# Kernel tuning notes

Hardware: AMD Instinct MI355X
Metric: run time of the kernel (lower is better)

Reference implementation:

```python
import jax, jax.numpy as jnp
import numpy as np

TEMPERATURE = 8.0  # sqrt(head_dim=64)
B, H, S, D = 4, 16, 2048, 64

def setup_inputs() -> dict:
    key = jax.random.key(0)
    kq, kk, kv, km = jax.random.split(key, 4)
    q = jax.random.normal(kq, (B, H, S, D), dtype=jnp.float32)
    k = jax.random.normal(kk, (B, H, S, D), dtype=jnp.float32)
    v = jax.random.normal(kv, (B, H, S, D), dtype=jnp.float32)
    # multiplicative 0/1 mask, broadcast over batch and heads
    mask = jax.random.randint(km, (1, 1, S, S), 0, 2).astype(jnp.float32)
    return {"q": q, "k": k, "v": v, "mask": mask}

def reference(q, k, v, mask):
    # attn = (q / T) @ k^T, multiplicatively masked, softmax over keys, then @ v
    attn = jnp.einsum("bhqd,bhkd->bhqk", q / TEMPERATURE, k)
    attn = attn * mask  # multiplicative mask (NOT additive -inf masking)
    attn = jax.nn.softmax(attn, axis=-1)
    return jnp.einsum("bhqk,bhkd->bhqd", attn, v)
```

## Files before the change

kernel.cpp:

```cpp
#include <hip/hip_runtime.h>
#include <hip/hip_bf16.h>


typedef __attribute__((ext_vector_type(4))) float  f32x4;
typedef __attribute__((ext_vector_type(8))) short  short8;
typedef __attribute__((ext_vector_type(4))) short  short4v;

constexpr int S = 2048, D = 64;
constexpr int NBH = 64;
constexpr int QBLK = 256, KT = 64;
constexpr int NQT = S / QBLK;
constexpr int NKT = S / KT;
constexpr float SCALE = 0.125f * 1.44269504088896340736f;
constexpr size_t TILE_SH = (size_t)KT * D;
constexpr size_t IMG_SH  = (size_t)NBH * NKT * TILE_SH;
constexpr size_t WS_NEED = 2 * IMG_SH * sizeof(short);

__device__ inline unsigned short bfb(float x) {
    union { __hip_bfloat16 h; unsigned short u; } cv;
    cv.h = __float2bfloat16(x);
    return cv.u;
}

__device__ inline float fexp2(float x) {
#if __has_builtin(__builtin_amdgcn_exp2f)
    return __builtin_amdgcn_exp2f(x);
#else
    return __expf(x * 0.6931471805599453f);
#endif
}

__device__ inline void gload16(const short* g, short* l) {
    auto gp = (const __attribute__((address_space(1))) int*)g;
    auto lp = (__attribute__((address_space(3))) int*)l;
    __builtin_amdgcn_global_load_lds(gp, lp, 16, 0, 0);
}

__global__ __launch_bounds__(256)
void conv_kv(const float* __restrict__ K, const float* __restrict__ V,
             short* __restrict__ Kimg, short* __restrict__ Vimg) {
    const int t = threadIdx.x;
    const int nt = NBH * NKT;
    if (blockIdx.x < nt) {
        const float* src = K + (size_t)blockIdx.x * TILE_SH;
        short* dst = Kimg + (size_t)blockIdx.x * TILE_SH;
        const int row = t >> 2, c16 = (t & 3) * 16;
        const int swz = (row & 7) << 3;
        float4 f0 = *reinterpret_cast<const float4*>(src + row * D + c16 + 0);
        float4 f1 = *reinterpret_cast<const float4*>(src + row * D + c16 + 4);
        float4 f2 = *reinterpret_cast<const float4*>(src + row * D + c16 + 8);
        float4 f3 = *reinterpret_cast<const float4*>(src + row * D + c16 + 12);
        short8 a, b;
        a[0]=bfb(f0.x); a[1]=bfb(f0.y); a[2]=bfb(f0.z); a[3]=bfb(f0.w);
        a[4]=bfb(f1.x); a[5]=bfb(f1.y); a[6]=bfb(f1.z); a[7]=bfb(f1.w);
        b[0]=bfb(f2.x); b[1]=bfb(f2.y); b[2]=bfb(f2.z); b[3]=bfb(f2.w);
        b[4]=bfb(f3.x); b[5]=bfb(f3.y); b[6]=bfb(f3.z); b[7]=bfb(f3.w);
        *reinterpret_cast<short8*>(dst + row * 64 + (c16 ^ swz)) = a;
        *reinterpret_cast<short8*>(dst + row * 64 + ((c16 + 8) ^ swz)) = b;
    } else {
        __shared__ float tl[64][65];
        const int blk = blockIdx.x - nt;
        const float* src = V + (size_t)blk * TILE_SH;
        short* dst = Vimg + (size_t)blk * TILE_SH;
        const int row = t >> 2, c16 = (t & 3) * 16;
        {
            float4 f0 = *reinterpret_cast<const float4*>(src + row * D + c16 + 0);
            float4 f1 = *reinterpret_cast<const float4*>(src + row * D + c16 + 4);
            float4 f2 = *reinterpret_cast<const float4*>(src + row * D + c16 + 8);
            float4 f3 = *reinterpret_cast<const float4*>(src + row * D + c16 + 12);
            tl[row][c16+0]=f0.x;  tl[row][c16+1]=f0.y;  tl[row][c16+2]=f0.z;  tl[row][c16+3]=f0.w;
            tl[row][c16+4]=f1.x;  tl[row][c16+5]=f1.y;  tl[row][c16+6]=f1.z;  tl[row][c16+7]=f1.w;
            tl[row][c16+8]=f2.x;  tl[row][c16+9]=f2.y;  tl[row][c16+10]=f2.z; tl[row][c16+11]=f2.w;
            tl[row][c16+12]=f3.x; tl[row][c16+13]=f3.y; tl[row][c16+14]=f3.z; tl[row][c16+15]=f3.w;
        }
        __syncthreads();
        const int d = t >> 2, k16 = (t & 3) * 16;
        const int swz = (d & 7) << 3;
        float vv[16];
#pragma unroll
        for (int j = 0; j < 16; ++j) vv[j] = tl[k16 + j][d];
        short8 a, b;
#pragma unroll
        for (int j = 0; j < 8; ++j) { a[j] = bfb(vv[j]); b[j] = bfb(vv[j + 8]); }
        *reinterpret_cast<short8*>(dst + d * 64 + (k16 ^ swz)) = a;
        *reinterpret_cast<short8*>(dst + d * 64 + ((k16 + 8) ^ swz)) = b;
    }
}

__global__ __launch_bounds__(512)
void attn_img(const float* __restrict__ Q, const float* __restrict__ M,
              const short* __restrict__ Kimg, const short* __restrict__ Vimg,
              float* __restrict__ O)
{
    __shared__ short Kb[3][4096];
    __shared__ short Vb[3][4096];
    __shared__ short Pt[8][16][64];

    const int tid  = threadIdx.x;
    const int w    = tid >> 6;
    const int lane = tid & 63;
    const int g    = lane >> 4;
    const int c    = lane & 15;
    const int swz8 = (c & 7) << 3;

    const int bid = blockIdx.x;
    const int bh  = bid >> 3;
    const int qt  = bid & 7;
    const int qw  = qt * QBLK + w * 32;

    const size_t bhS = (size_t)bh * S;
    const size_t bhT = (size_t)bh * NKT;

    short8 bQ[2][2];
#pragma unroll
    for (int rt = 0; rt < 2; ++rt) {
        const float* qp = Q + (bhS + qw + rt * 16 + c) * D;
#pragma unroll
        for (int kk = 0; kk < 2; ++kk) {
            const float* q8 = qp + kk * 32 + g * 8;
            float4 a = *reinterpret_cast<const float4*>(q8);
            float4 b = *reinterpret_cast<const float4*>(q8 + 4);
            short8 r;
            r[0] = bfb(a.x * SCALE); r[1] = bfb(a.y * SCALE);
            r[2] = bfb(a.z * SCALE); r[3] = bfb(a.w * SCALE);
            r[4] = bfb(b.x * SCALE); r[5] = bfb(b.y * SCALE);
            r[6] = bfb(b.z * SCALE); r[7] = bfb(b.w * SCALE);
            bQ[rt][kk] = r;
        }
    }

    const float* mrow0 = M + (size_t)(qw + c) * S;
    const float* mrow1 = M + (size_t)(qw + 16 + c) * S;

    f32x4 acc[2][4] = {};
    float lR[2] = {0.f, 0.f};

    auto stage = [&](int buf, int kt) {
        const short* ks = Kimg + (bhT + kt) * TILE_SH + tid * 8;
        const short* vs = Vimg + (bhT + kt) * TILE_SH + tid * 8;
        gload16(ks, &Kb[buf][tid * 8]);
        gload16(vs, &Vb[buf][tid * 8]);
    };

    stage(0, 0);
    stage(1, 1);

    for (int kt = 0; kt < NKT; ++kt) {
        if (kt == NKT - 1) {
            asm volatile("s_waitcnt vmcnt(0)" ::: "memory");
        } else {
            asm volatile("s_waitcnt vmcnt(2)" ::: "memory");
        }
        __builtin_amdgcn_s_barrier();
        __builtin_amdgcn_sched_barrier(0);

        if (kt + 2 < NKT) stage((kt + 2) % 3, kt + 2);

        const short* Kt = Kb[kt % 3];
        const short* Vt = Vb[kt % 3];
        const int k0 = kt * KT;

        f32x4 s[2][4] = {};
#pragma unroll
        for (int kk = 0; kk < 2; ++kk) {
            short8 aK[4];
#pragma unroll
            for (int n = 0; n < 4; ++n)
                aK[n] = *reinterpret_cast<const short8*>(
                    &Kt[(n * 16 + c) * 64 + ((kk * 32 + g * 8) ^ swz8)]);
            __builtin_amdgcn_s_setprio(1);
#pragma unroll
            for (int n = 0; n < 4; ++n) {
                s[0][n] = __builtin_amdgcn_mfma_f32_16x16x32_bf16(
                    aK[n], bQ[0][kk], s[0][n], 0, 0, 0);
                s[1][n] = __builtin_amdgcn_mfma_f32_16x16x32_bf16(
                    aK[n], bQ[1][kk], s[1][n], 0, 0, 0);
            }
            __builtin_amdgcn_s_setprio(0);
        }

#pragma unroll
        for (int rt = 0; rt < 2; ++rt) {
            const float* mrow = rt ? mrow1 : mrow0;

            float lp = 0.f;
#pragma unroll
            for (int n = 0; n < 4; ++n) {
                float4 mk = *reinterpret_cast<const float4*>(mrow + k0 + n * 16 + g * 4);
                float e0 = fexp2(s[rt][n][0] * mk.x);
                float e1 = fexp2(s[rt][n][1] * mk.y);
                float e2 = fexp2(s[rt][n][2] * mk.z);
                float e3 = fexp2(s[rt][n][3] * mk.w);
                lp += (e0 + e1) + (e2 + e3);
                short4v pk;
                pk[0] = bfb(e0); pk[1] = bfb(e1); pk[2] = bfb(e2); pk[3] = bfb(e3);
                *reinterpret_cast<short4v*>(
                    &Pt[w][c][(n * 16 + g * 4) ^ swz8]) = pk;
            }
            lR[rt] += lp;

#pragma unroll
            for (int kk = 0; kk < 2; ++kk) {
                short8 aP = *reinterpret_cast<const short8*>(
                    &Pt[w][c][(kk * 32 + g * 8) ^ swz8]);
                __builtin_amdgcn_s_setprio(1);
#pragma unroll
                for (int n = 0; n < 4; ++n) {
                    short8 bV = *reinterpret_cast<const short8*>(
                        &Vt[(n * 16 + c) * 64 + ((kk * 32 + g * 8) ^ swz8)]);
                    acc[rt][n] = __builtin_amdgcn_mfma_f32_16x16x32_bf16(
                        aP, bV, acc[rt][n], 0, 0, 0);
                }
                __builtin_amdgcn_s_setprio(0);
            }
        }
    }

#pragma unroll
    for (int rt = 0; rt < 2; ++rt) {
        float l = lR[rt];
        l += __shfl_xor(l, 16);
        l += __shfl_xor(l, 32);
        const float linv = 1.0f / l;
        float ld[4];
        ld[0] = __shfl(linv, 4 * g + 0);
        ld[1] = __shfl(linv, 4 * g + 1);
        ld[2] = __shfl(linv, 4 * g + 2);
        ld[3] = __shfl(linv, 4 * g + 3);
#pragma unroll
        for (int r = 0; r < 4; ++r) {
            float* op = O + (bhS + qw + rt * 16 + 4 * g + r) * D + c;
#pragma unroll
            for (int n = 0; n < 4; ++n) op[n * 16] = acc[rt][n][r] * ld[r];
        }
    }
}

constexpr int FQT = 256, FKT = 64, FSUB = 16;
__global__ __launch_bounds__(FQT)
void attn_f32(const float* __restrict__ Q, const float* __restrict__ K,
              const float* __restrict__ V, const float* __restrict__ M,
              float* __restrict__ O)
{
    __shared__ float Kt[FKT][D];
    __shared__ float Vt[FKT][D];
    const int tid = threadIdx.x;
    const int bh = blockIdx.x / (S / FQT);
    const int qrow = (blockIdx.x % (S / FQT)) * FQT + tid;
    const float* qp = Q + ((size_t)bh * S + qrow) * D;
    const float* mp = M + (size_t)qrow * S;
    const float* kb = K + (size_t)bh * S * D;
    const float* vb = V + (size_t)bh * S * D;
    float qv[D];
#pragma unroll
    for (int d = 0; d < D; d += 4) {
        float4 t = *reinterpret_cast<const float4*>(qp + d);
        qv[d] = t.x * 0.125f; qv[d+1] = t.y * 0.125f; qv[d+2] = t.z * 0.125f; qv[d+3] = t.w * 0.125f;
    }
    float acc[D];
#pragma unroll
    for (int d = 0; d < D; ++d) acc[d] = 0.f;
    float mrun = -1e30f, lrun = 0.f;
    for (int k0 = 0; k0 < S; k0 += FKT) {
        __syncthreads();
        const float4* ks = reinterpret_cast<const float4*>(kb + (size_t)k0 * D);
        const float4* vs = reinterpret_cast<const float4*>(vb + (size_t)k0 * D);
        float4* kd = reinterpret_cast<float4*>(&Kt[0][0]);
        float4* vd = reinterpret_cast<float4*>(&Vt[0][0]);
#pragma unroll
        for (int i = 0; i < (FKT * D / 4) / FQT; ++i) {
            kd[tid + FQT * i] = ks[tid + FQT * i];
            vd[tid + FQT * i] = vs[tid + FQT * i];
        }
        __syncthreads();
        for (int j0 = 0; j0 < FKT; j0 += FSUB) {
            float mk[FSUB];
#pragma unroll
            for (int i = 0; i < FSUB; i += 4) {
                float4 t = *reinterpret_cast<const float4*>(mp + k0 + j0 + i);
                mk[i] = t.x; mk[i+1] = t.y; mk[i+2] = t.z; mk[i+3] = t.w;
            }
            float sx[FSUB];
#pragma unroll
            for (int j = 0; j < FSUB; ++j) sx[j] = 0.f;
#pragma unroll
            for (int d = 0; d < D; d += 4)
#pragma unroll
                for (int j = 0; j < FSUB; ++j) {
                    float4 kv = *reinterpret_cast<const float4*>(&Kt[j0 + j][d]);
                    sx[j] = fmaf(qv[d], kv.x, sx[j]);
                    sx[j] = fmaf(qv[d+1], kv.y, sx[j]);
                    sx[j] = fmaf(qv[d+2], kv.z, sx[j]);
                    sx[j] = fmaf(qv[d+3], kv.w, sx[j]);
                }
            float cmax = -1e30f;
#pragma unroll
            for (int j = 0; j < FSUB; ++j) { sx[j] *= mk[j]; cmax = fmaxf(cmax, sx[j]); }
            if (cmax > mrun) {
                float r = __expf(mrun - cmax);
                mrun = cmax; lrun *= r;
#pragma unroll
                for (int d = 0; d < D; ++d) acc[d] *= r;
            }
#pragma unroll
            for (int j = 0; j < FSUB; ++j) {
                float p = __expf(sx[j] - mrun);
                lrun += p;
#pragma unroll
                for (int d = 0; d < D; d += 4) {
                    float4 vv = *reinterpret_cast<const float4*>(&Vt[j0 + j][d]);
                    acc[d] = fmaf(p, vv.x, acc[d]);
                    acc[d+1] = fmaf(p, vv.y, acc[d+1]);
                    acc[d+2] = fmaf(p, vv.z, acc[d+2]);
                    acc[d+3] = fmaf(p, vv.w, acc[d+3]);
                }
            }
        }
    }
    const float invl = 1.0f / lrun;
    float* op = O + ((size_t)bh * S + qrow) * D;
#pragma unroll
    for (int d = 0; d < D; d += 4) {
        float4 t;
        t.x = acc[d] * invl; t.y = acc[d+1] * invl; t.z = acc[d+2] * invl; t.w = acc[d+3] * invl;
        *reinterpret_cast<float4*>(op + d) = t;
    }
}

extern "C" void kernel_launch(void* const* d_in, const int* in_sizes, int n_in,
                              void* d_out, int out_size, void* d_ws, size_t ws_size,
                              hipStream_t stream) {
    const float* q = (const float*)d_in[0];
    const float* k = (const float*)d_in[1];
    const float* v = (const float*)d_in[2];
    const float* m = (const float*)d_in[3];
    float* out = (float*)d_out;
    if (ws_size >= WS_NEED) {
        short* kimg = (short*)d_ws;
        short* vimg = kimg + IMG_SH;
        conv_kv<<<dim3(2 * NBH * NKT), dim3(256), 0, stream>>>(k, v, kimg, vimg);
        attn_img<<<dim3(NBH * NQT), dim3(512), 0, stream>>>(q, m, kimg, vimg, out);
    } else {
        attn_f32<<<dim3(NBH * (S / FQT)), dim3(256), 0, stream>>>(q, k, v, m, out);
    }
}
```

Before: 159.4 us.

## Software-pipeline QK of next tile with softmax and PV of current tile

Restructures the main loop so the QK^T MFMAs for key tile kt+1 are issued between the softmax and PV phases of tile kt, interleaving the two row-tiles' work. The aim is to overlap the exponential/VALU softmax work with matrix-core work within each wave. To support this, the P staging buffer in LDS is doubled so both row tiles have separate storage, and an extra barrier is added per iteration. The extra barrier, more live registers and larger LDS footprint could reduce occupancy or add sync cost.

```diff
diff --git a/kernel.cpp b/kernel.cpp
--- a/kernel.cpp
+++ b/kernel.cpp
@@ -94,7 +94,7 @@
 {
     __shared__ short Kb[3][4096];
     __shared__ short Vb[3][4096];
-    __shared__ short Pt[8][16][64];
+    __shared__ short Pt[8][32][64];
 
     const int tid  = threadIdx.x;
     const int w    = tid >> 6;
@@ -142,25 +142,9 @@
         gload16(vs, &Vb[buf][tid * 8]);
     };
 
-    stage(0, 0);
-    stage(1, 1);
-
-    for (int kt = 0; kt < NKT; ++kt) {
-        if (kt == NKT - 1) {
-            asm volatile("s_waitcnt vmcnt(0)" ::: "memory");
-        } else {
-            asm volatile("s_waitcnt vmcnt(2)" ::: "memory");
-        }
-        __builtin_amdgcn_s_barrier();
-        __builtin_amdgcn_sched_barrier(0);
-
-        if (kt + 2 < NKT) stage((kt + 2) % 3, kt + 2);
-
-        const short* Kt = Kb[kt % 3];
-        const short* Vt = Vb[kt % 3];
-        const int k0 = kt * KT;
-
-        f32x4 s[2][4] = {};
+    auto qk = [&](const short* Kt, const short8 (&bq)[2], f32x4 (&s)[4]) {
+#pragma unroll
+        for (int n = 0; n < 4; ++n) s[n] = (f32x4){0.f, 0.f, 0.f, 0.f};
 #pragma unroll
         for (int kk = 0; kk < 2; ++kk) {
             short8 aK[4];
@@ -170,50 +154,78 @@
                     &Kt[(n * 16 + c) * 64 + ((kk * 32 + g * 8) ^ swz8)]);
             __builtin_amdgcn_s_setprio(1);
 #pragma unroll
+            for (int n = 0; n < 4; ++n)
+                s[n] = __builtin_amdgcn_mfma_f32_16x16x32_bf16(aK[n], bq[kk], s[n], 0, 0, 0);
+            __builtin_amdgcn_s_setprio(0);
+        }
+    };
+
+    auto softmax = [&](int rt, const float* mrow, int k0, f32x4 (&s)[4]) {
+        float lp = 0.f;
+#pragma unroll
+        for (int n = 0; n < 4; ++n) {
+            float4 mk = *reinterpret_cast<const float4*>(mrow + k0 + n * 16 + g * 4);
+            float e0 = fexp2(s[n][0] * mk.x);
+            float e1 = fexp2(s[n][1] * mk.y);
+            float e2 = fexp2(s[n][2] * mk.z);
+            float e3 = fexp2(s[n][3] * mk.w);
+            lp += (e0 + e1) + (e2 + e3);
+            short4v pk;
+            pk[0] = bfb(e0); pk[1] = bfb(e1); pk[2] = bfb(e2); pk[3] = bfb(e3);
+            *reinterpret_cast<short4v*>(
+                &Pt[w][rt * 16 + c][(n * 16 + g * 4) ^ swz8]) = pk;
+        }
+        lR[rt] += lp;
+    };
+
+    auto pv = [&](int rt, const short* Vt) {
+#pragma unroll
+        for (int kk = 0; kk < 2; ++kk) {
+            short8 aP = *reinterpret_cast<const short8*>(
+                &Pt[w][rt * 16 + c][(kk * 32 + g * 8) ^ swz8]);
+            __builtin_amdgcn_s_setprio(1);
+#pragma unroll
             for (int n = 0; n < 4; ++n) {
-                s[0][n] = __builtin_amdgcn_mfma_f32_16x16x32_bf16(
-                    aK[n], bQ[0][kk], s[0][n], 0, 0, 0);
-                s[1][n] = __builtin_amdgcn_mfma_f32_16x16x32_bf16(
-                    aK[n], bQ[1][kk], s[1][n], 0, 0, 0);
+                short8 bV = *reinterpret_cast<const short8*>(
+                    &Vt[(n * 16 + c) * 64 + ((kk * 32 + g * 8) ^ swz8)]);
+                acc[rt][n] = __builtin_amdgcn_mfma_f32_16x16x32_bf16(
+                    aP, bV, acc[rt][n], 0, 0, 0);
             }
             __builtin_amdgcn_s_setprio(0);
         }
-
-#pragma unroll
-        for (int rt = 0; rt < 2; ++rt) {
-            const float* mrow = rt ? mrow1 : mrow0;
-
-            float lp = 0.f;
-#pragma unroll
-            for (int n = 0; n < 4; ++n) {
-                float4 mk = *reinterpret_cast<const float4*>(mrow + k0 + n * 16 + g * 4);
-                float e0 = fexp2(s[rt][n][0] * mk.x);
-                float e1 = fexp2(s[rt][n][1] * mk.y);
-                float e2 = fexp2(s[rt][n][2] * mk.z);
-                float e3 = fexp2(s[rt][n][3] * mk.w);
-                lp += (e0 + e1) + (e2 + e3);
-                short4v pk;
-                pk[0] = bfb(e0); pk[1] = bfb(e1); pk[2] = bfb(e2); pk[3] = bfb(e3);
-                *reinterpret_cast<short4v*>(
-                    &Pt[w][c][(n * 16 + g * 4) ^ swz8]) = pk;
-            }
-            lR[rt] += lp;
-
-#pragma unroll
-            for (int kk = 0; kk < 2; ++kk) {
-                short8 aP = *reinterpret_cast<const short8*>(
-                    &Pt[w][c][(kk * 32 + g * 8) ^ swz8]);
-                __builtin_amdgcn_s_setprio(1);
-#pragma unroll
-                for (int n = 0; n < 4; ++n) {
-                    short8 bV = *reinterpret_cast<const short8*>(
-                        &Vt[(n * 16 + c) * 64 + ((kk * 32 + g * 8) ^ swz8)]);
-                    acc[rt][n] = __builtin_amdgcn_mfma_f32_16x16x32_bf16(
-                        aP, bV, acc[rt][n], 0, 0, 0);
-                }
-                __builtin_amdgcn_s_setprio(0);
-            }
-        }
+    };
+
+    stage(0, 0);
+    stage(1, 1);
+    asm volatile("s_waitcnt vmcnt(2)" ::: "memory");
+    __builtin_amdgcn_s_barrier();
+    __builtin_amdgcn_sched_barrier(0);
+
+    f32x4 sA[4], sB[4];
+    qk(Kb[0], bQ[0], sA);
+    qk(Kb[0], bQ[1], sB);
+
+    for (int kt = 0; kt < NKT; ++kt) {
+        __builtin_amdgcn_s_barrier();
+        if (kt + 2 < NKT) {
+            stage((kt + 2) % 3, kt + 2);
+            asm volatile("s_waitcnt vmcnt(2)" ::: "memory");
+        } else {
+            asm volatile("s_waitcnt vmcnt(0)" ::: "memory");
+        }
+        __builtin_amdgcn_s_barrier();
+        __builtin_amdgcn_sched_barrier(0);
+
+        const short* Ktn = Kb[(kt + 1) % 3];
+        const short* Vt  = Vb[kt % 3];
+        const int k0 = kt * KT;
+
+        softmax(0, mrow0, k0, sA);
+        if (kt + 1 < NKT) qk(Ktn, bQ[0], sA);
+        softmax(1, mrow1, k0, sB);
+        pv(0, Vt);
+        if (kt + 1 < NKT) qk(Ktn, bQ[1], sB);
+        pv(1, Vt);
     }
 
 #pragma unroll
```

Result: slower. 208.0 us (+30.4%).

## Switch attention to 32x32x16 MFMA and pass P through registers via lane shuffles

Applied to the files above, without the earlier changes.

Replaces the 16x16x32 bf16 MFMA tiling with 32x32x16 MFMAs, computing S^T so that each lane holds one query row's probabilities. The P matrix is repacked for the PV MFMA using cross-half lane shuffles instead of a round trip through an LDS staging buffer. This removes the Pt shared-memory writes and reads and cuts the MFMA instruction count. It also lets the mask be loaded once per row. In exchange it adds shuffle and select instructions and changes the output store pattern, and the larger accumulators may raise register pressure.

```diff
diff --git a/kernel.cpp b/kernel.cpp
--- a/kernel.cpp
+++ b/kernel.cpp
@@ -2,9 +2,10 @@
 #include <hip/hip_bf16.h>
 
 
-typedef __attribute__((ext_vector_type(4))) float  f32x4;
-typedef __attribute__((ext_vector_type(8))) short  short8;
-typedef __attribute__((ext_vector_type(4))) short  short4v;
+typedef __attribute__((ext_vector_type(4)))  float  f32x4;
+typedef __attribute__((ext_vector_type(16))) float  f32x16;
+typedef __attribute__((ext_vector_type(8)))  short  short8;
+typedef __attribute__((ext_vector_type(4)))  int    int4v;
 
 constexpr int S = 2048, D = 64;
 constexpr int NBH = 64;
@@ -94,14 +95,13 @@
 {
     __shared__ short Kb[3][4096];
     __shared__ short Vb[3][4096];
-    __shared__ short Pt[8][16][64];
 
     const int tid  = threadIdx.x;
     const int w    = tid >> 6;
     const int lane = tid & 63;
-    const int g    = lane >> 4;
-    const int c    = lane & 15;
-    const int swz8 = (c & 7) << 3;
+    const int c32  = lane & 31;
+    const int lo   = lane >> 5;
+    const int zr   = (c32 & 7) << 3;
 
     const int bid = blockIdx.x;
     const int bh  = bid >> 3;
@@ -111,13 +111,12 @@
     const size_t bhS = (size_t)bh * S;
     const size_t bhT = (size_t)bh * NKT;
 
-    short8 bQ[2][2];
-#pragma unroll
-    for (int rt = 0; rt < 2; ++rt) {
-        const float* qp = Q + (bhS + qw + rt * 16 + c) * D;
-#pragma unroll
-        for (int kk = 0; kk < 2; ++kk) {
-            const float* q8 = qp + kk * 32 + g * 8;
+    short8 bQ[4];
+    {
+        const float* qp = Q + (bhS + qw + c32) * D;
+#pragma unroll
+        for (int ks = 0; ks < 4; ++ks) {
+            const float* q8 = qp + ks * 16 + lo * 8;
             float4 a = *reinterpret_cast<const float4*>(q8);
             float4 b = *reinterpret_cast<const float4*>(q8 + 4);
             short8 r;
@@ -125,15 +124,14 @@
             r[2] = bfb(a.z * SCALE); r[3] = bfb(a.w * SCALE);
             r[4] = bfb(b.x * SCALE); r[5] = bfb(b.y * SCALE);
             r[6] = bfb(b.z * SCALE); r[7] = bfb(b.w * SCALE);
-            bQ[rt][kk] = r;
-        }
-    }
-
-    const float* mrow0 = M + (size_t)(qw + c) * S;
-    const float* mrow1 = M + (size_t)(qw + 16 + c) * S;
-
-    f32x4 acc[2][4] = {};
-    float lR[2] = {0.f, 0.f};
+            bQ[ks] = r;
+        }
+    }
+
+    const float* mrow = M + (size_t)(qw + c32) * S;
+
+    f32x16 acc32[2] = {};
+    float lR = 0.f;
 
     auto stage = [&](int buf, int kt) {
         const short* ks = Kimg + (bhT + kt) * TILE_SH + tid * 8;
@@ -160,78 +158,73 @@
         const short* Vt = Vb[kt % 3];
         const int k0 = kt * KT;
 
-        f32x4 s[2][4] = {};
-#pragma unroll
-        for (int kk = 0; kk < 2; ++kk) {
-            short8 aK[4];
-#pragma unroll
-            for (int n = 0; n < 4; ++n)
-                aK[n] = *reinterpret_cast<const short8*>(
-                    &Kt[(n * 16 + c) * 64 + ((kk * 32 + g * 8) ^ swz8)]);
+        f32x16 sT[2] = {};
+        __builtin_amdgcn_s_setprio(1);
+#pragma unroll
+        for (int ks = 0; ks < 4; ++ks) {
+            short8 a0 = *reinterpret_cast<const short8*>(
+                &Kt[c32 * 64 + ((ks * 16 + lo * 8) ^ zr)]);
+            short8 a1 = *reinterpret_cast<const short8*>(
+                &Kt[(c32 + 32) * 64 + ((ks * 16 + lo * 8) ^ zr)]);
+            sT[0] = __builtin_amdgcn_mfma_f32_32x32x16_bf16(a0, bQ[ks], sT[0], 0, 0, 0);
+            sT[1] = __builtin_amdgcn_mfma_f32_32x32x16_bf16(a1, bQ[ks], sT[1], 0, 0, 0);
+        }
+        __builtin_amdgcn_s_setprio(0);
+
+        unsigned prx[2][4], pry[2][4];
+        float lp = 0.f;
+#pragma unroll
+        for (int sub = 0; sub < 2; ++sub) {
+#pragma unroll
+            for (int q = 0; q < 4; ++q) {
+                float4 mk = *reinterpret_cast<const float4*>(
+                    mrow + k0 + 32 * sub + 8 * q + 4 * lo);
+                float e0 = fexp2(sT[sub][4 * q + 0] * mk.x);
+                float e1 = fexp2(sT[sub][4 * q + 1] * mk.y);
+                float e2 = fexp2(sT[sub][4 * q + 2] * mk.z);
+                float e3 = fexp2(sT[sub][4 * q + 3] * mk.w);
+                lp += (e0 + e1) + (e2 + e3);
+                prx[sub][q] = (unsigned)bfb(e0) | ((unsigned)bfb(e1) << 16);
+                pry[sub][q] = (unsigned)bfb(e2) | ((unsigned)bfb(e3) << 16);
+            }
+        }
+        lR += lp;
+
+#pragma unroll
+        for (int kk = 0; kk < 4; ++kk) {
+            const int sub = kk >> 1, b = kk & 1;
+            const unsigned ux = prx[sub][2 * b],     uy = pry[sub][2 * b];
+            const unsigned vx = prx[sub][2 * b + 1], vy = pry[sub][2 * b + 1];
+            const unsigned sx = lo ? ux : vx, sy = lo ? uy : vy;
+            const unsigned rx = __shfl_xor(sx, 32), ry = __shfl_xor(sy, 32);
+            int4v f;
+            f.x = (int)(lo ? rx : ux);
+            f.y = (int)(lo ? ry : uy);
+            f.z = (int)(lo ? vx : rx);
+            f.w = (int)(lo ? vy : ry);
+            short8 aP = *reinterpret_cast<short8*>(&f);
             __builtin_amdgcn_s_setprio(1);
 #pragma unroll
-            for (int n = 0; n < 4; ++n) {
-                s[0][n] = __builtin_amdgcn_mfma_f32_16x16x32_bf16(
-                    aK[n], bQ[0][kk], s[0][n], 0, 0, 0);
-                s[1][n] = __builtin_amdgcn_mfma_f32_16x16x32_bf16(
-                    aK[n], bQ[1][kk], s[1][n], 0, 0, 0);
+            for (int n = 0; n < 2; ++n) {
+                const int vr = c32 + 32 * n;
+                short8 bV = *reinterpret_cast<const short8*>(
+                    &Vt[vr * 64 + ((kk * 16 + lo * 8) ^ zr)]);
+                acc32[n] = __builtin_amdgcn_mfma_f32_32x32x16_bf16(aP, bV, acc32[n], 0, 0, 0);
             }
             __builtin_amdgcn_s_setprio(0);
         }
-
-#pragma unroll
-        for (int rt = 0; rt < 2; ++rt) {
-            const float* mrow = rt ? mrow1 : mrow0;
-
-            float lp = 0.f;
-#pragma unroll
-            for (int n = 0; n < 4; ++n) {
-                float4 mk = *reinterpret_cast<const float4*>(mrow + k0 + n * 16 + g * 4);
-                float e0 = fexp2(s[rt][n][0] * mk.x);
-                float e1 = fexp2(s[rt][n][1] * mk.y);
-                float e2 = fexp2(s[rt][n][2] * mk.z);
-                float e3 = fexp2(s[rt][n][3] * mk.w);
-                lp += (e0 + e1) + (e2 + e3);
-                short4v pk;
-                pk[0] = bfb(e0); pk[1] = bfb(e1); pk[2] = bfb(e2); pk[3] = bfb(e3);
-                *reinterpret_cast<short4v*>(
-                    &Pt[w][c][(n * 16 + g * 4) ^ swz8]) = pk;
-            }
-            lR[rt] += lp;
-
-#pragma unroll
-            for (int kk = 0; kk < 2; ++kk) {
-                short8 aP = *reinterpret_cast<const short8*>(
-                    &Pt[w][c][(kk * 32 + g * 8) ^ swz8]);
-                __builtin_amdgcn_s_setprio(1);
-#pragma unroll
-                for (int n = 0; n < 4; ++n) {
-                    short8 bV = *reinterpret_cast<const short8*>(
-                        &Vt[(n * 16 + c) * 64 + ((kk * 32 + g * 8) ^ swz8)]);
-                    acc[rt][n] = __builtin_amdgcn_mfma_f32_16x16x32_bf16(
-                        aP, bV, acc[rt][n], 0, 0, 0);
-                }
-                __builtin_amdgcn_s_setprio(0);
-            }
-        }
-    }
-
-#pragma unroll
-    for (int rt = 0; rt < 2; ++rt) {
-        float l = lR[rt];
-        l += __shfl_xor(l, 16);
-        l += __shfl_xor(l, 32);
+    }
+
+    {
+        const float l = lR + __shfl_xor(lR, 32);
         const float linv = 1.0f / l;
-        float ld[4];
-        ld[0] = __shfl(linv, 4 * g + 0);
-        ld[1] = __shfl(linv, 4 * g + 1);
-        ld[2] = __shfl(linv, 4 * g + 2);
-        ld[3] = __shfl(linv, 4 * g + 3);
-#pragma unroll
-        for (int r = 0; r < 4; ++r) {
-            float* op = O + (bhS + qw + rt * 16 + 4 * g + r) * D + c;
-#pragma unroll
-            for (int n = 0; n < 4; ++n) op[n * 16] = acc[rt][n][r] * ld[r];
+#pragma unroll
+        for (int j = 0; j < 16; ++j) {
+            const int qrow = (j & 3) + 8 * (j >> 2) + 4 * lo;
+            const float ldv = __shfl(linv, qrow);
+            float* op = O + (bhS + qw + qrow) * D + c32;
+            op[0]  = acc32[0][j] * ldv;
+            op[32] = acc32[1][j] * ldv;
         }
     }
 }
```

Result: slower. 180.1 us (+12.9%).
